# Performance work log

Hardware: AMD Instinct MI355X
Metric: run time of the kernel (lower is better)

Reference implementation:

```python
import jax, jax.numpy as jnp
import numpy as np

B, T, D = 8, 2048, 1024  # batch, seq (== block_size), n_embd == head_size


def setup_inputs() -> dict:
    key = jax.random.key(0)
    k0, k1, k2, k3 = jax.random.split(key, 4)
    s = 1.0 / np.sqrt(D)
    return {
        "x": jax.random.normal(k0, (B, T, D), dtype=jnp.float32),
        "Wk": jax.random.normal(k1, (D, D), dtype=jnp.float32) * s,
        "Wq": jax.random.normal(k2, (D, D), dtype=jnp.float32) * s,
        "Wv": jax.random.normal(k3, (D, D), dtype=jnp.float32) * s,
    }


def reference(x, Wk, Wq, Wv):
    Bb, Tt, C = x.shape
    k = jnp.einsum("btc,ch->bth", x, Wk)
    q = jnp.einsum("btc,ch->bth", x, Wq)
    v = jnp.einsum("btc,ch->bth", x, Wv)
    # scaled dot-product scores with causal (tril) mask; scale = C**-0.5 (n_embd)
    wei = jnp.einsum("bqh,bkh->bqk", q, k) * (1.0 / jnp.sqrt(jnp.float32(C)))
    causal = jnp.tril(jnp.ones((Tt, Tt), dtype=bool))
    wei = jnp.where(causal[None, :, :], wei, jnp.float32(-jnp.inf))
    wei = jax.nn.softmax(wei, axis=-1)
    # dropout is identity in eval mode
    out = jnp.einsum("bqk,bkh->bqh", wei, v)
    return out
```

## Files before the change

### kernel.cpp

```cpp
#include <hip/hip_runtime.h>
#include <hip/hip_bf16.h>

#define BB 8
#define TT 2048
#define DD 1024

typedef __attribute__((ext_vector_type(8))) short short8;
typedef __attribute__((ext_vector_type(4))) float f32x4;
typedef __attribute__((ext_vector_type(4))) unsigned short u16x4;

__device__ inline void gload_lds16(const void* g, void* l) {
    __builtin_amdgcn_global_load_lds((const __attribute__((address_space(1))) void*)g,
                                     (__attribute__((address_space(3))) void*)l, 16, 0, 0);
}

template<int MODE, typename CT>
__device__ __forceinline__ void gemm_core(
    const __hip_bfloat16* __restrict__ A,
    const __hip_bfloat16* __restrict__ Bt,
    void* __restrict__ Cbase,
    int lda, int ldb, int ldc,
    int m0, int n0, int kmax,
    float scale, float* __restrict__ rs)
{
    __shared__ __align__(16) __hip_bfloat16 lsA[128 * 64];
    __shared__ __align__(16) __hip_bfloat16 lsB[128 * 64];

    const int t    = threadIdx.x;
    const int w    = t >> 6;
    const int l    = t & 63;
    const int quad = l >> 4;
    const int l16  = l & 15;
    const int wy   = w >> 1;
    const int wx   = w & 1;

    f32x4 acc[4][4];
#pragma unroll
    for (int i = 0; i < 4; i++)
#pragma unroll
        for (int j = 0; j < 4; j++) acc[i][j] = f32x4{0.f, 0.f, 0.f, 0.f};

    for (int k0 = 0; k0 < kmax; k0 += 64) {
#pragma unroll
        for (int p = 0; p < 4; p++) {
            int c   = p * 256 + t;
            int row = c >> 3;
            int gch = (c & 7) ^ (row & 7);
            const __hip_bfloat16* ga = A  + (size_t)(m0 + row) * lda + (k0 + gch * 8);
            const __hip_bfloat16* gb = Bt + (size_t)(n0 + row) * ldb + (k0 + gch * 8);
            char* la = (char*)lsA + p * 4096 + w * 1024;
            char* lb = (char*)lsB + p * 4096 + w * 1024;
            gload_lds16(ga, la);
            gload_lds16(gb, lb);
        }
        __syncthreads();

#pragma unroll
        for (int h = 0; h < 2; h++) {
            short8 aF[4], bF[4];
#pragma unroll
            for (int mf = 0; mf < 4; mf++) {
                int m = wy * 64 + mf * 16 + l16;
                aF[mf] = *(const short8*)((const char*)lsA + m * 128 +
                                          (((h * 4 + quad) ^ (m & 7)) * 16));
            }
#pragma unroll
            for (int nf = 0; nf < 4; nf++) {
                int n = wx * 64 + nf * 16 + l16;
                bF[nf] = *(const short8*)((const char*)lsB + n * 128 +
                                          (((h * 4 + quad) ^ (n & 7)) * 16));
            }
#pragma unroll
            for (int mf = 0; mf < 4; mf++)
#pragma unroll
                for (int nf = 0; nf < 4; nf++)
                    acc[mf][nf] = __builtin_amdgcn_mfma_f32_16x16x32_bf16(
                        aF[mf], bF[nf], acc[mf][nf], 0, 0, 0);
        }
        __syncthreads();
    }

    if constexpr (MODE == 0) {
        CT* C = (CT*)Cbase;
#pragma unroll
        for (int mf = 0; mf < 4; mf++) {
            int rbase = m0 + wy * 64 + mf * 16 + quad * 4;
#pragma unroll
            for (int nf = 0; nf < 4; nf++) {
                int col = n0 + wx * 64 + nf * 16 + l16;
#pragma unroll
                for (int r = 0; r < 4; r++) {
                    float v = acc[mf][nf][r] * scale;
                    if constexpr (sizeof(CT) == 2)
                        C[(size_t)(rbase + r) * ldc + col] = (CT)__float2bfloat16(v);
                    else
                        *((float*)&C[(size_t)(rbase + r) * ldc + col]) = v;
                }
            }
        }
    } else if constexpr (MODE == 1) {
        __hip_bfloat16* C = (__hip_bfloat16*)Cbase;
#pragma unroll
        for (int mf = 0; mf < 4; mf++) {
            int rbase = m0 + wy * 64 + mf * 16 + quad * 4;
#pragma unroll
            for (int r = 0; r < 4; r++) {
                int row = rbase + r;
                float part = 0.f, pv[4];
#pragma unroll
                for (int nf = 0; nf < 4; nf++) {
                    int col = n0 + wx * 64 + nf * 16 + l16;
                    float e = (col <= row) ? __expf(acc[mf][nf][r] * scale) : 0.f;
                    pv[nf] = e;
                    part += e;
                }
                part += __shfl_xor(part, 1, 64);
                part += __shfl_xor(part, 2, 64);
                part += __shfl_xor(part, 4, 64);
                part += __shfl_xor(part, 8, 64);
                if (l16 == 0) atomicAdd(&rs[row], part);
#pragma unroll
                for (int nf = 0; nf < 4; nf++) {
                    int col = n0 + wx * 64 + nf * 16 + l16;
                    C[(size_t)row * ldc + col] = __float2bfloat16(pv[nf]);
                }
            }
        }
    } else {
        float* C = (float*)Cbase;
#pragma unroll
        for (int mf = 0; mf < 4; mf++) {
            int rbase = m0 + wy * 64 + mf * 16 + quad * 4;
#pragma unroll
            for (int r = 0; r < 4; r++) {
                int row = rbase + r;
                float inv = 1.f / rs[row];
#pragma unroll
                for (int nf = 0; nf < 4; nf++) {
                    int col = n0 + wx * 64 + nf * 16 + l16;
                    C[(size_t)row * ldc + col] = acc[mf][nf][r] * inv;
                }
            }
        }
    }
}

__global__ __launch_bounds__(256, 3) void proj3(
    const __hip_bfloat16* __restrict__ xb,
    const __hip_bfloat16* __restrict__ wt,
    __hip_bfloat16* __restrict__ kq,
    __hip_bfloat16* __restrict__ vT2)
{
    const int z = blockIdx.z;
    const __hip_bfloat16 *A, *Bt;
    void* C;
    int ldc, m0, n0;
    if (z < 2) {
        A = xb; Bt = wt + z * 1048576; C = kq + (size_t)z * 16777216;
        ldc = 1024; m0 = blockIdx.x * 128; n0 = blockIdx.y * 128;
    } else {
        A = wt + 2 * 1048576; Bt = xb; C = vT2;
        ldc = 16384; m0 = blockIdx.y * 128; n0 = blockIdx.x * 128;
    }
    gemm_core<0, __hip_bfloat16>(A, Bt, C, 1024, 1024, ldc, m0, n0, 1024, 1.0f, nullptr);
}

template<int MODE, typename CT>
__global__ __launch_bounds__(256, 3) void gemm_bt(
    const __hip_bfloat16* __restrict__ Abase,
    const __hip_bfloat16* __restrict__ Btbase,
    void* __restrict__ Cbase,
    int K, int lda, int ldb, int ldc,
    long long sA, long long sB, long long sC,
    float scale, int causalSkip, int causalKStop, int swapMN, int permX,
    float* __restrict__ aux)
{
    int bx = blockIdx.x;
    if (permX) bx = (bx < 8) ? 15 - bx : bx - 8;
    const int m0 = (swapMN ? bx : blockIdx.y) * 128;
    const int n0 = (swapMN ? blockIdx.y : bx) * 128;
    if (causalSkip && n0 > m0) return;

    const int z = blockIdx.z;
    int kmax = K;
    if (causalKStop) { int km = m0 + 128; kmax = km < K ? km : K; }

    gemm_core<MODE, CT>(Abase + (size_t)z * sA, Btbase + (size_t)z * sB,
                        (char*)Cbase + (size_t)z * sC * sizeof(CT),
                        lda, ldb, ldc, m0, n0, kmax, scale,
                        aux ? aux + (size_t)z * TT : nullptr);
}

__global__ __launch_bounds__(256) void cvt_x(const float* __restrict__ in,
                                             unsigned short* __restrict__ out)
{
    size_t i = ((size_t)blockIdx.x * 256 + threadIdx.x) * 4;
    float4 f = *(const float4*)(in + i);
    union { u16x4 u; __hip_bfloat16 h[4]; } o;
    o.h[0] = __float2bfloat16(f.x);
    o.h[1] = __float2bfloat16(f.y);
    o.h[2] = __float2bfloat16(f.z);
    o.h[3] = __float2bfloat16(f.w);
    *(u16x4*)(out + i) = o.u;
}

__global__ __launch_bounds__(256) void transpose_cvt_w(
    const float* __restrict__ Wk, const float* __restrict__ Wq,
    const float* __restrict__ Wv, __hip_bfloat16* __restrict__ Wt)
{
    const float* W = blockIdx.z == 0 ? Wk : (blockIdx.z == 1 ? Wq : Wv);
    __hip_bfloat16* o = Wt + (size_t)blockIdx.z * DD * DD;
    int h0 = blockIdx.x * 32, c0 = blockIdx.y * 32;
    __shared__ float tl[32][33];
    int tx = threadIdx.x, ty = threadIdx.y;
#pragma unroll
    for (int k = 0; k < 4; k++)
        tl[ty + 8 * k][tx] = W[(size_t)(c0 + ty + 8 * k) * DD + h0 + tx];
    __syncthreads();
#pragma unroll
    for (int k = 0; k < 4; k++)
        o[(size_t)(h0 + ty + 8 * k) * DD + c0 + tx] = __float2bfloat16(tl[tx][ty + 8 * k]);
}

extern "C" void kernel_launch(void* const* d_in, const int* in_sizes, int n_in,
                              void* d_out, int out_size, void* d_ws, size_t ws_size,
                              hipStream_t stream)
{
    const float* x  = (const float*)d_in[0];
    const float* Wk = (const float*)d_in[1];
    const float* Wq = (const float*)d_in[2];
    const float* Wv = (const float*)d_in[3];
    float* out = (float*)d_out;

    char* ws = (char*)d_ws;
    __hip_bfloat16* kk   = (__hip_bfloat16*)ws;
    __hip_bfloat16* qq   = (__hip_bfloat16*)(ws + 33554432);
    __hip_bfloat16* vT2  = (__hip_bfloat16*)(ws + 67108864);
    __hip_bfloat16* wt   = (__hip_bfloat16*)(ws + 100663296);
    float*          rsum = (float*)         (ws + 100663296);
    __hip_bfloat16* xb   = (__hip_bfloat16*)(ws + 106954752);
    __hip_bfloat16* Pp   = (__hip_bfloat16*)(ws + 106954752);

    int g = (ws_size >= 106954752ull + 8ull * 8388608ull) ? 8 : 4;

    cvt_x<<<16384, 256, 0, stream>>>(x, (unsigned short*)xb);
    transpose_cvt_w<<<dim3(32, 32, 3), dim3(32, 8), 0, stream>>>(Wk, Wq, Wv, wt);

    proj3<<<dim3(128, 8, 3), 256, 0, stream>>>(xb, wt, kk, vT2);

    for (int g0 = 0; g0 < BB; g0 += g) {
        hipMemsetAsync(rsum, 0, (size_t)g * TT * 4, stream);

        gemm_bt<1, __hip_bfloat16><<<dim3(16, 16, g), 256, 0, stream>>>(
            qq + (size_t)g0 * 2097152, kk + (size_t)g0 * 2097152, (void*)Pp,
            1024, 1024, 1024, 2048,
            2097152LL, 2097152LL, 4194304LL, 0.03125f, 1, 0, 0, 1, rsum);

        gemm_bt<2, float><<<dim3(16, 8, g), 256, 0, stream>>>(
            Pp, vT2 + (size_t)g0 * 2048, (void*)(out + (size_t)g0 * 2097152),
            2048, 2048, 16384, 1024,
            4194304LL, 2048LL, 2097152LL, 1.0f, 0, 1, 1, 1, rsum);
    }
}
```

Measured before the change: 362.2 us.

## Move all GEMMs to 256x256 tiles with double-buffered LDS pipeline

Replaces the 128x128 single-buffered GEMM core with a 256x256-tile core using 512 threads, 128 KB of double-buffered LDS and split-K half-steps. Global-to-LDS loads for the next tile are interleaved with MFMA pairs under explicit vmcnt waits and barriers, with setprio raised around the MFMA bursts. Projection blocks get a swizzled tile order for cache locality. The aim is more data reuse per byte loaded and overlap of memory with compute. In exchange, the larger tiles mean coarser causal skipping, fewer blocks in flight, and higher register and LDS pressure. The 128 KB of LDS per block may also limit occupancy to one block per CU, below the launch bound's target of two.

```diff
diff --git a/kernel.cpp b/kernel.cpp
--- a/kernel.cpp
+++ b/kernel.cpp
@@ -14,8 +14,25 @@
                                      (__attribute__((address_space(3))) void*)l, 16, 0, 0);
 }
 
+#define VMW4 asm volatile("s_waitcnt vmcnt(4)" ::: "memory")
+#define VMW0 asm volatile("s_waitcnt vmcnt(0)" ::: "memory")
+#define BARX() __builtin_amdgcn_s_barrier()
+
+#define MM_PAIR(NF0)                                                          \
+    do {                                                                      \
+        __builtin_amdgcn_s_setprio(1);                                        \
+        _Pragma("unroll")                                                     \
+        for (int mf = 0; mf < 8; mf++) {                                      \
+            acc[mf][NF0] = __builtin_amdgcn_mfma_f32_16x16x32_bf16(           \
+                aF[mf], bF[NF0], acc[mf][NF0], 0, 0, 0);                      \
+            acc[mf][NF0 + 1] = __builtin_amdgcn_mfma_f32_16x16x32_bf16(       \
+                aF[mf], bF[NF0 + 1], acc[mf][NF0 + 1], 0, 0, 0);              \
+        }                                                                     \
+        __builtin_amdgcn_s_setprio(0);                                        \
+    } while (0)
+
 template<int MODE, typename CT>
-__device__ __forceinline__ void gemm_core(
+__device__ __forceinline__ void gemm_core256(
     const __hip_bfloat16* __restrict__ A,
     const __hip_bfloat16* __restrict__ Bt,
     void* __restrict__ Cbase,
@@ -23,71 +40,100 @@
     int m0, int n0, int kmax,
     float scale, float* __restrict__ rs)
 {
-    __shared__ __align__(16) __hip_bfloat16 lsA[128 * 64];
-    __shared__ __align__(16) __hip_bfloat16 lsB[128 * 64];
-
-    const int t    = threadIdx.x;
-    const int w    = t >> 6;
-    const int l    = t & 63;
-    const int quad = l >> 4;
-    const int l16  = l & 15;
-    const int wy   = w >> 1;
-    const int wx   = w & 1;
-
-    f32x4 acc[4][4];
-#pragma unroll
-    for (int i = 0; i < 4; i++)
-#pragma unroll
-        for (int j = 0; j < 4; j++) acc[i][j] = f32x4{0.f, 0.f, 0.f, 0.f};
-
-    for (int k0 = 0; k0 < kmax; k0 += 64) {
-#pragma unroll
-        for (int p = 0; p < 4; p++) {
-            int c   = p * 256 + t;
-            int row = c >> 3;
-            int gch = (c & 7) ^ (row & 7);
-            const __hip_bfloat16* ga = A  + (size_t)(m0 + row) * lda + (k0 + gch * 8);
-            const __hip_bfloat16* gb = Bt + (size_t)(n0 + row) * ldb + (k0 + gch * 8);
-            char* la = (char*)lsA + p * 4096 + w * 1024;
-            char* lb = (char*)lsB + p * 4096 + w * 1024;
-            gload_lds16(ga, la);
-            gload_lds16(gb, lb);
-        }
-        __syncthreads();
-
-#pragma unroll
-        for (int h = 0; h < 2; h++) {
-            short8 aF[4], bF[4];
-#pragma unroll
-            for (int mf = 0; mf < 4; mf++) {
-                int m = wy * 64 + mf * 16 + l16;
-                aF[mf] = *(const short8*)((const char*)lsA + m * 128 +
-                                          (((h * 4 + quad) ^ (m & 7)) * 16));
-            }
-#pragma unroll
-            for (int nf = 0; nf < 4; nf++) {
-                int n = wx * 64 + nf * 16 + l16;
-                bF[nf] = *(const short8*)((const char*)lsB + n * 128 +
-                                          (((h * 4 + quad) ^ (n & 7)) * 16));
-            }
-#pragma unroll
-            for (int mf = 0; mf < 4; mf++)
-#pragma unroll
-                for (int nf = 0; nf < 4; nf++)
-                    acc[mf][nf] = __builtin_amdgcn_mfma_f32_16x16x32_bf16(
-                        aF[mf], bF[nf], acc[mf][nf], 0, 0, 0);
-        }
-        __syncthreads();
+    __shared__ __align__(16) char lsA[65536];
+    __shared__ __align__(16) char lsB[65536];
+
+    const int t   = threadIdx.x;
+    const int w   = t >> 6;
+    const int l   = t & 63;
+    const int q   = l >> 4;
+    const int i16 = l & 15;
+    const int wy  = w >> 2;
+    const int wx  = w & 3;
+
+    const int r0  = w * 32 + (l >> 2);
+    const int r1  = r0 + 16;
+    const int cg0 = (l & 3) ^ ((r0 >> 1) & 3);
+    const int cg1 = (l & 3) ^ ((r1 >> 1) & 3);
+    const __hip_bfloat16* gA0 = A  + (size_t)(m0 + r0) * lda + cg0 * 8;
+    const __hip_bfloat16* gA1 = A  + (size_t)(m0 + r1) * lda + cg1 * 8;
+    const __hip_bfloat16* gB0 = Bt + (size_t)(n0 + r0) * ldb + cg0 * 8;
+    const __hip_bfloat16* gB1 = Bt + (size_t)(n0 + r1) * ldb + cg1 * 8;
+
+    const int swz  = (q ^ ((i16 >> 1) & 3)) << 4;
+    const int offA = (wy * 128 + i16) * 64 + swz;
+    const int offB = (wx * 64  + i16) * 64 + swz;
+
+    f32x4 acc[8][4];
+#pragma unroll
+    for (int mf = 0; mf < 8; mf++)
+#pragma unroll
+        for (int nf = 0; nf < 4; nf++) acc[mf][nf] = f32x4{0.f, 0.f, 0.f, 0.f};
+
+    short8 aF[8], bF[4];
+    const int NT = kmax >> 6;
+
+    {
+        char* dA = lsA + (w << 11);
+        char* dB = lsB + (w << 11);
+        gload_lds16(gA0, dA);            gload_lds16(gA1, dA + 1024);
+        gload_lds16(gB0, dB);            gload_lds16(gB1, dB + 1024);
+        gload_lds16(gA0 + 32, dA + 16384); gload_lds16(gA1 + 32, dA + 16384 + 1024);
+        gload_lds16(gB0 + 32, dB + 16384); gload_lds16(gB1 + 32, dB + 16384 + 1024);
+    }
+    VMW4; BARX();
+
+    int buf = 0;
+    for (int tt = 0; tt < NT; ++tt, buf ^= 1) {
+        const bool nx = (tt + 1) < NT;
+        const int  kn = (tt + 1) << 6;
+        char* sA = lsA + (buf ? 32768 : 0);
+        char* sB = lsB + (buf ? 32768 : 0);
+        char* dA = lsA + (buf ? 0 : 32768) + (w << 11);
+        char* dB = lsB + (buf ? 0 : 32768) + (w << 11);
+
+#pragma unroll
+        for (int mf = 0; mf < 8; mf++)
+            aF[mf] = *(const short8*)(sA + offA + mf * 1024);
+#pragma unroll
+        for (int nf = 0; nf < 4; nf++)
+            bF[nf] = *(const short8*)(sB + offB + nf * 1024);
+        if (nx) { gload_lds16(gA0 + kn, dA); gload_lds16(gA1 + kn, dA + 1024); }
+        BARX();
+        MM_PAIR(0);
+        BARX();
+        if (nx) { gload_lds16(gB0 + kn, dB); gload_lds16(gB1 + kn, dB + 1024); }
+        BARX();
+        MM_PAIR(2);
+        if (nx) { VMW4; } else { VMW0; }
+        BARX();
+#pragma unroll
+        for (int mf = 0; mf < 8; mf++)
+            aF[mf] = *(const short8*)(sA + 16384 + offA + mf * 1024);
+#pragma unroll
+        for (int nf = 0; nf < 4; nf++)
+            bF[nf] = *(const short8*)(sB + 16384 + offB + nf * 1024);
+        if (nx) { gload_lds16(gA0 + kn + 32, dA + 16384);
+                  gload_lds16(gA1 + kn + 32, dA + 16384 + 1024); }
+        BARX();
+        MM_PAIR(0);
+        BARX();
+        if (nx) { gload_lds16(gB0 + kn + 32, dB + 16384);
+                  gload_lds16(gB1 + kn + 32, dB + 16384 + 1024); }
+        BARX();
+        MM_PAIR(2);
+        if (nx) { VMW4; }
+        BARX();
     }
 
     if constexpr (MODE == 0) {
         CT* C = (CT*)Cbase;
 #pragma unroll
-        for (int mf = 0; mf < 4; mf++) {
-            int rbase = m0 + wy * 64 + mf * 16 + quad * 4;
+        for (int mf = 0; mf < 8; mf++) {
+            int rbase = m0 + wy * 128 + mf * 16 + q * 4;
 #pragma unroll
             for (int nf = 0; nf < 4; nf++) {
-                int col = n0 + wx * 64 + nf * 16 + l16;
+                int col = n0 + wx * 64 + nf * 16 + i16;
 #pragma unroll
                 for (int r = 0; r < 4; r++) {
                     float v = acc[mf][nf][r] * scale;
@@ -101,15 +147,15 @@
     } else if constexpr (MODE == 1) {
         __hip_bfloat16* C = (__hip_bfloat16*)Cbase;
 #pragma unroll
-        for (int mf = 0; mf < 4; mf++) {
-            int rbase = m0 + wy * 64 + mf * 16 + quad * 4;
+        for (int mf = 0; mf < 8; mf++) {
+            int rbase = m0 + wy * 128 + mf * 16 + q * 4;
 #pragma unroll
             for (int r = 0; r < 4; r++) {
                 int row = rbase + r;
                 float part = 0.f, pv[4];
 #pragma unroll
                 for (int nf = 0; nf < 4; nf++) {
-                    int col = n0 + wx * 64 + nf * 16 + l16;
+                    int col = n0 + wx * 64 + nf * 16 + i16;
                     float e = (col <= row) ? __expf(acc[mf][nf][r] * scale) : 0.f;
                     pv[nf] = e;
                     part += e;
@@ -118,10 +164,10 @@
                 part += __shfl_xor(part, 2, 64);
                 part += __shfl_xor(part, 4, 64);
                 part += __shfl_xor(part, 8, 64);
-                if (l16 == 0) atomicAdd(&rs[row], part);
+                if (i16 == 0) atomicAdd(&rs[row], part);
 #pragma unroll
                 for (int nf = 0; nf < 4; nf++) {
-                    int col = n0 + wx * 64 + nf * 16 + l16;
+                    int col = n0 + wx * 64 + nf * 16 + i16;
                     C[(size_t)row * ldc + col] = __float2bfloat16(pv[nf]);
                 }
             }
@@ -129,15 +175,15 @@
     } else {
         float* C = (float*)Cbase;
 #pragma unroll
-        for (int mf = 0; mf < 4; mf++) {
-            int rbase = m0 + wy * 64 + mf * 16 + quad * 4;
+        for (int mf = 0; mf < 8; mf++) {
+            int rbase = m0 + wy * 128 + mf * 16 + q * 4;
 #pragma unroll
             for (int r = 0; r < 4; r++) {
                 int row = rbase + r;
                 float inv = 1.f / rs[row];
 #pragma unroll
                 for (int nf = 0; nf < 4; nf++) {
-                    int col = n0 + wx * 64 + nf * 16 + l16;
+                    int col = n0 + wx * 64 + nf * 16 + i16;
                     C[(size_t)row * ldc + col] = acc[mf][nf][r] * inv;
                 }
             }
@@ -145,50 +191,59 @@
     }
 }
 
-__global__ __launch_bounds__(256, 3) void proj3(
+__global__ __launch_bounds__(512, 2) void proj3_8ph(
     const __hip_bfloat16* __restrict__ xb,
     const __hip_bfloat16* __restrict__ wt,
     __hip_bfloat16* __restrict__ kq,
     __hip_bfloat16* __restrict__ vT2)
 {
-    const int z = blockIdx.z;
+    const int z = blockIdx.y;
+    const int x = blockIdx.x;
+    const int swz = (x & 7) * 32 + (x >> 3);
     const __hip_bfloat16 *A, *Bt;
     void* C;
     int ldc, m0, n0;
     if (z < 2) {
         A = xb; Bt = wt + z * 1048576; C = kq + (size_t)z * 16777216;
-        ldc = 1024; m0 = blockIdx.x * 128; n0 = blockIdx.y * 128;
+        ldc = 1024; m0 = (swz >> 2) * 256; n0 = (swz & 3) * 256;
     } else {
         A = wt + 2 * 1048576; Bt = xb; C = vT2;
-        ldc = 16384; m0 = blockIdx.y * 128; n0 = blockIdx.x * 128;
-    }
-    gemm_core<0, __hip_bfloat16>(A, Bt, C, 1024, 1024, ldc, m0, n0, 1024, 1.0f, nullptr);
-}
-
-template<int MODE, typename CT>
-__global__ __launch_bounds__(256, 3) void gemm_bt(
-    const __hip_bfloat16* __restrict__ Abase,
-    const __hip_bfloat16* __restrict__ Btbase,
-    void* __restrict__ Cbase,
-    int K, int lda, int ldb, int ldc,
-    long long sA, long long sB, long long sC,
-    float scale, int causalSkip, int causalKStop, int swapMN, int permX,
-    float* __restrict__ aux)
-{
-    int bx = blockIdx.x;
-    if (permX) bx = (bx < 8) ? 15 - bx : bx - 8;
-    const int m0 = (swapMN ? bx : blockIdx.y) * 128;
-    const int n0 = (swapMN ? blockIdx.y : bx) * 128;
-    if (causalSkip && n0 > m0) return;
-
+        ldc = 16384; m0 = (swz & 3) * 256; n0 = (swz >> 2) * 256;
+    }
+    gemm_core256<0, __hip_bfloat16>(A, Bt, C, 1024, 1024, ldc, m0, n0, 1024, 1.0f, nullptr);
+}
+
+__global__ __launch_bounds__(512, 2) void sgemm256(
+    const __hip_bfloat16* __restrict__ qq,
+    const __hip_bfloat16* __restrict__ kk,
+    __hip_bfloat16* __restrict__ Pp,
+    float* __restrict__ rsum)
+{
     const int z = blockIdx.z;
-    int kmax = K;
-    if (causalKStop) { int km = m0 + 128; kmax = km < K ? km : K; }
-
-    gemm_core<MODE, CT>(Abase + (size_t)z * sA, Btbase + (size_t)z * sB,
-                        (char*)Cbase + (size_t)z * sC * sizeof(CT),
-                        lda, ldb, ldc, m0, n0, kmax, scale,
-                        aux ? aux + (size_t)z * TT : nullptr);
+    const int y = blockIdx.y;
+    const int ne = ((y + z) & 1) ? blockIdx.x : 7 - blockIdx.x;
+    if (ne > y) return;
+    gemm_core256<1, __hip_bfloat16>(
+        qq + (size_t)z * 2097152, kk + (size_t)z * 2097152,
+        Pp + (size_t)z * 4194304,
+        1024, 1024, 2048, y * 256, ne * 256, 1024, 0.03125f,
+        rsum + (size_t)z * TT);
+}
+
+__global__ __launch_bounds__(512, 2) void pvgemm256(
+    const __hip_bfloat16* __restrict__ Pp,
+    const __hip_bfloat16* __restrict__ vT2,
+    float* __restrict__ out,
+    float* __restrict__ rsum)
+{
+    const int z = blockIdx.z;
+    const int y = blockIdx.y;
+    const int x = blockIdx.x;
+    gemm_core256<2, float>(
+        Pp + (size_t)z * 4194304, vT2 + (size_t)z * 2048,
+        out + (size_t)z * 2097152,
+        2048, 16384, 1024, y * 256, x * 256, (y + 1) * 256, 1.0f,
+        rsum + (size_t)z * TT);
 }
 
 __global__ __launch_bounds__(256) void cvt_x(const float* __restrict__ in,
@@ -246,19 +301,15 @@
     cvt_x<<<16384, 256, 0, stream>>>(x, (unsigned short*)xb);
     transpose_cvt_w<<<dim3(32, 32, 3), dim3(32, 8), 0, stream>>>(Wk, Wq, Wv, wt);
 
-    proj3<<<dim3(128, 8, 3), 256, 0, stream>>>(xb, wt, kk, vT2);
+    proj3_8ph<<<dim3(256, 3), 512, 0, stream>>>(xb, wt, kk, vT2);
 
     for (int g0 = 0; g0 < BB; g0 += g) {
         hipMemsetAsync(rsum, 0, (size_t)g * TT * 4, stream);
 
-        gemm_bt<1, __hip_bfloat16><<<dim3(16, 16, g), 256, 0, stream>>>(
-            qq + (size_t)g0 * 2097152, kk + (size_t)g0 * 2097152, (void*)Pp,
-            1024, 1024, 1024, 2048,
-            2097152LL, 2097152LL, 4194304LL, 0.03125f, 1, 0, 0, 1, rsum);
-
-        gemm_bt<2, float><<<dim3(16, 8, g), 256, 0, stream>>>(
-            Pp, vT2 + (size_t)g0 * 2048, (void*)(out + (size_t)g0 * 2097152),
-            2048, 2048, 16384, 1024,
-            4194304LL, 2048LL, 2097152LL, 1.0f, 0, 1, 1, 1, rsum);
-    }
-}
+        sgemm256<<<dim3(8, 8, g), 512, 0, stream>>>(
+            qq + (size_t)g0 * 2097152, kk + (size_t)g0 * 2097152, Pp, rsum);
+
+        pvgemm256<<<dim3(4, 8, g), 512, 0, stream>>>(
+            Pp, vT2 + (size_t)g0 * 2048, out + (size_t)g0 * 2097152, rsum);
+    }
+}
```

Result: no change. 369.4 us (+2.0%).
